# Performance work log

Measured on AMD Instinct MI355X. Metric: run time of the kernel, lower is better.

The kernel has to match this reference:

```python
import jax, jax.numpy as jnp
import numpy as np


def setup_inputs() -> dict:
    key = jax.random.key(0)
    k1, k2, k3 = jax.random.split(key, 3)
    B, C, K, W, H = 8, 512, 512, 64, 64
    x = jax.random.normal(k1, (B, C, W, H), dtype=jnp.float32)
    y = jax.random.normal(k2, (B, K, W, H), dtype=jnp.float32)
    scale = jax.random.uniform(k3, (1,), dtype=jnp.float32)
    return {"x": x, "y": y, "scale": scale}


def reference(x, y, scale):
    B, C, W, H = x.shape
    K = y.shape[1]
    xq = x.reshape(B, C, W * H)            # [B, C, N]
    yk = y.reshape(B, K, W * H)            # [B, K, N]
    # energy = Q @ K^T : [B, C, K]
    energy = jnp.einsum('bcn,bkn->bck', xq, yk)
    # inverted max-subtract softmax over last dim (K)
    energy_new = jnp.max(energy, axis=-1, keepdims=True) - energy
    attention = jax.nn.softmax(energy_new, axis=-1)  # [B, C, K]
    # out = attention @ V : [B, C, N]
    out = jnp.einsum('bck,bkn->bcn', attention, yk).reshape(B, C, W, H)
    return x + scale * out
```

## Files before the change

### kernel.cpp

```cpp
#include <hip/hip_runtime.h>
#include <hip/hip_bf16.h>
#include <stdint.h>

#define BB 8
#define CC 512
#define KK 512
#define NN 4096

typedef __bf16 bf16x8 __attribute__((ext_vector_type(8)));
typedef float f32x4 __attribute__((ext_vector_type(4)));
typedef __attribute__((address_space(3))) uint8_t* lds_ptr_t;
typedef const __attribute__((address_space(1))) uint8_t* gbl_ptr_t;

static __device__ __forceinline__ unsigned short bf16_bits(float f) {
    __bf16 h = (__bf16)f;
    return __builtin_bit_cast(unsigned short, h);
}

__global__ void __launch_bounds__(256) split_hi_lo(const float* __restrict__ in,
        unsigned short* __restrict__ hi, unsigned short* __restrict__ lo, int n4) {
    int idx = blockIdx.x * blockDim.x + threadIdx.x;
    int stride = gridDim.x * blockDim.x;
    const float4* in4 = (const float4*)in;
    ushort4* h4 = (ushort4*)hi;
    ushort4* l4 = (ushort4*)lo;
    for (int i = idx; i < n4; i += stride) {
        float4 v = in4[i];
        float a[4] = {v.x, v.y, v.z, v.w};
        unsigned short hb[4], lb[4];
        #pragma unroll
        for (int j = 0; j < 4; ++j) {
            __bf16 h = (__bf16)a[j];
            float hf = (float)h;
            __bf16 l = (__bf16)(a[j] - hf);
            hb[j] = __builtin_bit_cast(unsigned short, h);
            lb[j] = __builtin_bit_cast(unsigned short, l);
        }
        h4[i] = make_ushort4(hb[0], hb[1], hb[2], hb[3]);
        l4[i] = make_ushort4(lb[0], lb[1], lb[2], lb[3]);
    }
}

__global__ void __launch_bounds__(256) energy_gemm(
        const unsigned short* __restrict__ xh, const unsigned short* __restrict__ xl,
        const unsigned short* __restrict__ yh, const unsigned short* __restrict__ yl,
        float* __restrict__ energy) {
    __shared__ __align__(16) uint8_t smem[4 * 8192];
    const int ktile = blockIdx.x;
    const int ctile = blockIdx.y;
    const int b = blockIdx.z >> 1;
    const int half = blockIdx.z & 1;
    const int t = threadIdx.x;
    const int wave = t >> 6, lane = t & 63;

    const size_t rowB = (size_t)NN * 2;
    const uint8_t* srcBase[4];
    srcBase[0] = (const uint8_t*)xh + ((size_t)b * CC + ctile * 64) * rowB + (size_t)half * 4096;
    srcBase[1] = (const uint8_t*)xl + ((size_t)b * CC + ctile * 64) * rowB + (size_t)half * 4096;
    srcBase[2] = (const uint8_t*)yh + ((size_t)b * KK + ktile * 64) * rowB + (size_t)half * 4096;
    srcBase[3] = (const uint8_t*)yl + ((size_t)b * KK + ktile * 64) * rowB + (size_t)half * 4096;

    f32x4 acc[2][2] = {};
    const int waveRow = wave >> 1, waveCol = wave & 1;

    for (int step = 0; step < 32; ++step) {
        const size_t colByte = (size_t)step * 128;
        #pragma unroll
        for (int i = 0; i < 8; ++i) {
            const int tile = i >> 1;
            const int lc = (i & 1) * 4 + wave;
            const int u = lc * 64 + lane;
            const int r = u >> 3;
            const int c3 = (u & 7) ^ (r & 7);
            const uint8_t* src = srcBase[tile] + (size_t)r * rowB + colByte + c3 * 16;
            __builtin_amdgcn_global_load_lds((gbl_ptr_t)src,
                (lds_ptr_t)(smem + tile * 8192 + lc * 1024), 16, 0, 0);
        }
        __syncthreads();
        #pragma unroll
        for (int kf = 0; kf < 2; ++kf) {
            bf16x8 fah[2], fal[2], fbh[2], fbl[2];
            #pragma unroll
            for (int m = 0; m < 2; ++m) {
                int r = waveRow * 32 + m * 16 + (lane & 15);
                int c3 = (kf * 4 + (lane >> 4)) ^ (r & 7);
                fah[m] = *(const bf16x8*)(smem + 0 * 8192 + r * 128 + c3 * 16);
                fal[m] = *(const bf16x8*)(smem + 1 * 8192 + r * 128 + c3 * 16);
            }
            #pragma unroll
            for (int n = 0; n < 2; ++n) {
                int r = waveCol * 32 + n * 16 + (lane & 15);
                int c3 = (kf * 4 + (lane >> 4)) ^ (r & 7);
                fbh[n] = *(const bf16x8*)(smem + 2 * 8192 + r * 128 + c3 * 16);
                fbl[n] = *(const bf16x8*)(smem + 3 * 8192 + r * 128 + c3 * 16);
            }
            #pragma unroll
            for (int m = 0; m < 2; ++m)
            #pragma unroll
            for (int n = 0; n < 2; ++n) {
                acc[m][n] = __builtin_amdgcn_mfma_f32_16x16x32_bf16(fah[m], fbh[n], acc[m][n], 0, 0, 0);
                acc[m][n] = __builtin_amdgcn_mfma_f32_16x16x32_bf16(fah[m], fbl[n], acc[m][n], 0, 0, 0);
                acc[m][n] = __builtin_amdgcn_mfma_f32_16x16x32_bf16(fal[m], fbh[n], acc[m][n], 0, 0, 0);
            }
        }
        __syncthreads();
    }

    float* eout = energy + (size_t)half * BB * CC * KK + (size_t)b * CC * KK;
    const int row0 = ctile * 64 + waveRow * 32;
    const int col0 = ktile * 64 + waveCol * 32;
    #pragma unroll
    for (int m = 0; m < 2; ++m)
    #pragma unroll
    for (int n = 0; n < 2; ++n)
    #pragma unroll
    for (int j = 0; j < 4; ++j) {
        int rr = row0 + m * 16 + (lane >> 4) * 4 + j;
        int cc2 = col0 + n * 16 + (lane & 15);
        eout[(size_t)rr * KK + cc2] = acc[m][n][j];
    }
}

__global__ void __launch_bounds__(256) softmax_inv(
        const float* __restrict__ e0, const float* __restrict__ e1,
        unsigned short* __restrict__ att) {
    const int t = threadIdx.x;
    const int wave = t >> 6, lane = t & 63;
    const int row = blockIdx.x * 4 + wave;
    const float* p0 = e0 + (size_t)row * KK;
    const float* p1 = e1 + (size_t)row * KK;
    float v[8];
    float mn = 3.0e38f;
    #pragma unroll
    for (int i = 0; i < 8; ++i) {
        v[i] = p0[lane + i * 64] + p1[lane + i * 64];
        mn = fminf(mn, v[i]);
    }
    #pragma unroll
    for (int off = 32; off > 0; off >>= 1) mn = fminf(mn, __shfl_xor(mn, off));
    float p[8]; float s = 0.f;
    #pragma unroll
    for (int i = 0; i < 8; ++i) { p[i] = __expf(mn - v[i]); s += p[i]; }
    #pragma unroll
    for (int off = 32; off > 0; off >>= 1) s += __shfl_xor(s, off);
    float inv = 1.0f / s;
    unsigned short* arow = att + (size_t)row * KK;
    #pragma unroll
    for (int i = 0; i < 8; ++i) arow[lane + i * 64] = bf16_bits(p[i] * inv);
}

__global__ void __launch_bounds__(256) transpose_bf16(
        const unsigned short* __restrict__ yh, unsigned short* __restrict__ yT) {
    __shared__ unsigned short tile[64][66];
    const int n0 = blockIdx.x * 64, k0 = blockIdx.y * 64, b = blockIdx.z;
    const int t = threadIdx.x;
    const unsigned short* src = yh + (size_t)b * KK * NN;
    unsigned short* dst = yT + (size_t)b * NN * KK;
    #pragma unroll
    for (int i = 0; i < 2; ++i) {
        int idx = t + 256 * i;
        int r = idx >> 3;
        int c8 = (idx & 7) * 8;
        uint4 v = *(const uint4*)(src + (size_t)(k0 + r) * NN + n0 + c8);
        unsigned int w[4] = {v.x, v.y, v.z, v.w};
        #pragma unroll
        for (int q = 0; q < 4; ++q) {
            tile[r][c8 + 2 * q]     = (unsigned short)(w[q] & 0xffffu);
            tile[r][c8 + 2 * q + 1] = (unsigned short)(w[q] >> 16);
        }
    }
    __syncthreads();
    #pragma unroll
    for (int i = 0; i < 16; ++i) {
        int idx = t + 256 * i;
        int rn = idx >> 6;
        int ck = idx & 63;
        dst[(size_t)(n0 + rn) * KK + k0 + ck] = tile[ck][rn];
    }
}

__global__ void __launch_bounds__(256) pv_residual(
        const unsigned short* __restrict__ att, const unsigned short* __restrict__ yT,
        const float* __restrict__ x, const float* __restrict__ scale,
        float* __restrict__ out) {
    __shared__ __align__(16) uint8_t smem[2 * 16384];
    const int ntile = blockIdx.x;
    const int ctile = blockIdx.y;
    const int b = blockIdx.z;
    const int t = threadIdx.x;
    const int wave = t >> 6, lane = t & 63;
    const size_t rowB = (size_t)KK * 2;
    const uint8_t* srcA = (const uint8_t*)att + ((size_t)b * CC + ctile * 128) * rowB;
    const uint8_t* srcB = (const uint8_t*)yT  + ((size_t)b * NN + ntile * 128) * rowB;

    f32x4 acc[4][4] = {};
    const int waveRow = wave >> 1, waveCol = wave & 1;

    for (int step = 0; step < 8; ++step) {
        const size_t colByte = (size_t)step * 128;
        #pragma unroll
        for (int i = 0; i < 8; ++i) {
            const uint8_t* base = (i < 4) ? srcA : srcB;
            const int tile = i >> 2;
            const int lc = (i & 3) * 4 + wave;
            const int u = lc * 64 + lane;
            const int r = u >> 3;
            const int c3 = (u & 7) ^ (r & 7);
            const uint8_t* src = base + (size_t)r * rowB + colByte + c3 * 16;
            __builtin_amdgcn_global_load_lds((gbl_ptr_t)src,
                (lds_ptr_t)(smem + tile * 16384 + lc * 1024), 16, 0, 0);
        }
        __syncthreads();
        #pragma unroll
        for (int kf = 0; kf < 2; ++kf) {
            bf16x8 fa[4], fb[4];
            #pragma unroll
            for (int m = 0; m < 4; ++m) {
                int r = waveRow * 64 + m * 16 + (lane & 15);
                int c3 = (kf * 4 + (lane >> 4)) ^ (r & 7);
                fa[m] = *(const bf16x8*)(smem + r * 128 + c3 * 16);
            }
            #pragma unroll
            for (int n = 0; n < 4; ++n) {
                int r = waveCol * 64 + n * 16 + (lane & 15);
                int c3 = (kf * 4 + (lane >> 4)) ^ (r & 7);
                fb[n] = *(const bf16x8*)(smem + 16384 + r * 128 + c3 * 16);
            }
            #pragma unroll
            for (int m = 0; m < 4; ++m)
            #pragma unroll
            for (int n = 0; n < 4; ++n)
                acc[m][n] = __builtin_amdgcn_mfma_f32_16x16x32_bf16(fa[m], fb[n], acc[m][n], 0, 0, 0);
        }
        __syncthreads();
    }

    const float s = scale[0];
    const int row0 = ctile * 128 + waveRow * 64;
    const int col0 = ntile * 128 + waveCol * 64;
    #pragma unroll
    for (int m = 0; m < 4; ++m)
    #pragma unroll
    for (int n = 0; n < 4; ++n)
    #pragma unroll
    for (int j = 0; j < 4; ++j) {
        int rr = row0 + m * 16 + (lane >> 4) * 4 + j;
        int cc2 = col0 + n * 16 + (lane & 15);
        size_t idx = ((size_t)b * CC + rr) * NN + cc2;
        out[idx] = x[idx] + s * acc[m][n][j];
    }
}

extern "C" void kernel_launch(void* const* d_in, const int* in_sizes, int n_in,
                              void* d_out, int out_size, void* d_ws, size_t ws_size,
                              hipStream_t stream) {
    const float* x = (const float*)d_in[0];
    const float* y = (const float*)d_in[1];
    const float* scale = (const float*)d_in[2];
    float* out = (float*)d_out;
    uint8_t* ws = (uint8_t*)d_ws;
    const size_t MB = 1024 * 1024;
    unsigned short* xh = (unsigned short*)(ws + 0 * MB);
    unsigned short* xl = (unsigned short*)(ws + 32 * MB);
    unsigned short* yh = (unsigned short*)(ws + 64 * MB);
    unsigned short* yl = (unsigned short*)(ws + 96 * MB);
    float* energy = (float*)(ws + 128 * MB);
    unsigned short* yT  = (unsigned short*)(ws + 0 * MB);
    unsigned short* att = (unsigned short*)(ws + 32 * MB);

    const int n4 = BB * CC * NN / 4;
    split_hi_lo<<<4096, 256, 0, stream>>>(x, xh, xl, n4);
    split_hi_lo<<<4096, 256, 0, stream>>>(y, yh, yl, n4);
    energy_gemm<<<dim3(8, 8, BB * 2), 256, 0, stream>>>(xh, xl, yh, yl, energy);
    transpose_bf16<<<dim3(NN / 64, KK / 64, BB), 256, 0, stream>>>(yh, yT);
    softmax_inv<<<dim3(BB * CC / 4), 256, 0, stream>>>(
        energy, energy + (size_t)BB * CC * KK, att);
    pv_residual<<<dim3(NN / 128, CC / 128, BB), 256, 0, stream>>>(att, yT, x, scale, out);
}
```

Before: 323.2 us.

## Enlarge energy GEMM tile to 128x128 with 4-way split-K into output buffer

The energy GEMM tile grows from 64x64 to 128x128 per block, with each wave computing a 64x64 sub-tile. This gives more MFMA work per LDS load and halves global reloads of the bf16 hi/lo operands. The reduction dimension is split four ways instead of two, and the partial sums are staged in the output buffer rather than a separate workspace. Softmax then sums the four partials. The grid has 512 blocks, each using 64KB of LDS and 64 accumulator registers, so occupancy may drop.

```diff
diff --git a/kernel.cpp b/kernel.cpp
--- a/kernel.cpp
+++ b/kernel.cpp
@@ -44,60 +44,60 @@
 __global__ void __launch_bounds__(256) energy_gemm(
         const unsigned short* __restrict__ xh, const unsigned short* __restrict__ xl,
         const unsigned short* __restrict__ yh, const unsigned short* __restrict__ yl,
-        float* __restrict__ energy) {
-    __shared__ __align__(16) uint8_t smem[4 * 8192];
+        float* __restrict__ epart) {
+    __shared__ __align__(16) uint8_t smem[4 * 16384];
     const int ktile = blockIdx.x;
     const int ctile = blockIdx.y;
-    const int b = blockIdx.z >> 1;
-    const int half = blockIdx.z & 1;
+    const int b = blockIdx.z >> 2;
+    const int quarter = blockIdx.z & 3;
     const int t = threadIdx.x;
     const int wave = t >> 6, lane = t & 63;
 
     const size_t rowB = (size_t)NN * 2;
     const uint8_t* srcBase[4];
-    srcBase[0] = (const uint8_t*)xh + ((size_t)b * CC + ctile * 64) * rowB + (size_t)half * 4096;
-    srcBase[1] = (const uint8_t*)xl + ((size_t)b * CC + ctile * 64) * rowB + (size_t)half * 4096;
-    srcBase[2] = (const uint8_t*)yh + ((size_t)b * KK + ktile * 64) * rowB + (size_t)half * 4096;
-    srcBase[3] = (const uint8_t*)yl + ((size_t)b * KK + ktile * 64) * rowB + (size_t)half * 4096;
-
-    f32x4 acc[2][2] = {};
+    srcBase[0] = (const uint8_t*)xh + ((size_t)b * CC + ctile * 128) * rowB + (size_t)quarter * 2048;
+    srcBase[1] = (const uint8_t*)xl + ((size_t)b * CC + ctile * 128) * rowB + (size_t)quarter * 2048;
+    srcBase[2] = (const uint8_t*)yh + ((size_t)b * KK + ktile * 128) * rowB + (size_t)quarter * 2048;
+    srcBase[3] = (const uint8_t*)yl + ((size_t)b * KK + ktile * 128) * rowB + (size_t)quarter * 2048;
+
+    f32x4 acc[4][4] = {};
     const int waveRow = wave >> 1, waveCol = wave & 1;
 
-    for (int step = 0; step < 32; ++step) {
+    for (int step = 0; step < 16; ++step) {
         const size_t colByte = (size_t)step * 128;
         #pragma unroll
-        for (int i = 0; i < 8; ++i) {
-            const int tile = i >> 1;
-            const int lc = (i & 1) * 4 + wave;
+        for (int i = 0; i < 16; ++i) {
+            const int tile = i >> 2;
+            const int lc = (i & 3) * 4 + wave;
             const int u = lc * 64 + lane;
             const int r = u >> 3;
             const int c3 = (u & 7) ^ (r & 7);
             const uint8_t* src = srcBase[tile] + (size_t)r * rowB + colByte + c3 * 16;
             __builtin_amdgcn_global_load_lds((gbl_ptr_t)src,
-                (lds_ptr_t)(smem + tile * 8192 + lc * 1024), 16, 0, 0);
+                (lds_ptr_t)(smem + tile * 16384 + lc * 1024), 16, 0, 0);
         }
         __syncthreads();
         #pragma unroll
         for (int kf = 0; kf < 2; ++kf) {
-            bf16x8 fah[2], fal[2], fbh[2], fbl[2];
-            #pragma unroll
-            for (int m = 0; m < 2; ++m) {
-                int r = waveRow * 32 + m * 16 + (lane & 15);
-                int c3 = (kf * 4 + (lane >> 4)) ^ (r & 7);
-                fah[m] = *(const bf16x8*)(smem + 0 * 8192 + r * 128 + c3 * 16);
-                fal[m] = *(const bf16x8*)(smem + 1 * 8192 + r * 128 + c3 * 16);
-            }
-            #pragma unroll
-            for (int n = 0; n < 2; ++n) {
-                int r = waveCol * 32 + n * 16 + (lane & 15);
-                int c3 = (kf * 4 + (lane >> 4)) ^ (r & 7);
-                fbh[n] = *(const bf16x8*)(smem + 2 * 8192 + r * 128 + c3 * 16);
-                fbl[n] = *(const bf16x8*)(smem + 3 * 8192 + r * 128 + c3 * 16);
-            }
-            #pragma unroll
-            for (int m = 0; m < 2; ++m)
-            #pragma unroll
-            for (int n = 0; n < 2; ++n) {
+            bf16x8 fah[4], fal[4], fbh[4], fbl[4];
+            #pragma unroll
+            for (int m = 0; m < 4; ++m) {
+                int r = waveRow * 64 + m * 16 + (lane & 15);
+                int c3 = (kf * 4 + (lane >> 4)) ^ (r & 7);
+                fah[m] = *(const bf16x8*)(smem + 0 * 16384 + r * 128 + c3 * 16);
+                fal[m] = *(const bf16x8*)(smem + 1 * 16384 + r * 128 + c3 * 16);
+            }
+            #pragma unroll
+            for (int n = 0; n < 4; ++n) {
+                int r = waveCol * 64 + n * 16 + (lane & 15);
+                int c3 = (kf * 4 + (lane >> 4)) ^ (r & 7);
+                fbh[n] = *(const bf16x8*)(smem + 2 * 16384 + r * 128 + c3 * 16);
+                fbl[n] = *(const bf16x8*)(smem + 3 * 16384 + r * 128 + c3 * 16);
+            }
+            #pragma unroll
+            for (int m = 0; m < 4; ++m)
+            #pragma unroll
+            for (int n = 0; n < 4; ++n) {
                 acc[m][n] = __builtin_amdgcn_mfma_f32_16x16x32_bf16(fah[m], fbh[n], acc[m][n], 0, 0, 0);
                 acc[m][n] = __builtin_amdgcn_mfma_f32_16x16x32_bf16(fah[m], fbl[n], acc[m][n], 0, 0, 0);
                 acc[m][n] = __builtin_amdgcn_mfma_f32_16x16x32_bf16(fal[m], fbh[n], acc[m][n], 0, 0, 0);
@@ -106,13 +106,13 @@
         __syncthreads();
     }
 
-    float* eout = energy + (size_t)half * BB * CC * KK + (size_t)b * CC * KK;
-    const int row0 = ctile * 64 + waveRow * 32;
-    const int col0 = ktile * 64 + waveCol * 32;
-    #pragma unroll
-    for (int m = 0; m < 2; ++m)
-    #pragma unroll
-    for (int n = 0; n < 2; ++n)
+    float* eout = epart + (size_t)quarter * BB * CC * KK + (size_t)b * CC * KK;
+    const int row0 = ctile * 128 + waveRow * 64;
+    const int col0 = ktile * 128 + waveCol * 64;
+    #pragma unroll
+    for (int m = 0; m < 4; ++m)
+    #pragma unroll
+    for (int n = 0; n < 4; ++n)
     #pragma unroll
     for (int j = 0; j < 4; ++j) {
         int rr = row0 + m * 16 + (lane >> 4) * 4 + j;
@@ -122,18 +122,18 @@
 }
 
 __global__ void __launch_bounds__(256) softmax_inv(
-        const float* __restrict__ e0, const float* __restrict__ e1,
-        unsigned short* __restrict__ att) {
+        const float* __restrict__ e, unsigned short* __restrict__ att) {
     const int t = threadIdx.x;
     const int wave = t >> 6, lane = t & 63;
     const int row = blockIdx.x * 4 + wave;
-    const float* p0 = e0 + (size_t)row * KK;
-    const float* p1 = e1 + (size_t)row * KK;
+    const size_t Q = (size_t)BB * CC * KK;
+    const float* p0 = e + (size_t)row * KK;
     float v[8];
     float mn = 3.0e38f;
     #pragma unroll
     for (int i = 0; i < 8; ++i) {
-        v[i] = p0[lane + i * 64] + p1[lane + i * 64];
+        int c = lane + i * 64;
+        v[i] = p0[c] + p0[Q + c] + p0[2 * Q + c] + p0[3 * Q + c];
         mn = fminf(mn, v[i]);
     }
     #pragma unroll
@@ -264,16 +264,15 @@
     unsigned short* xl = (unsigned short*)(ws + 32 * MB);
     unsigned short* yh = (unsigned short*)(ws + 64 * MB);
     unsigned short* yl = (unsigned short*)(ws + 96 * MB);
-    float* energy = (float*)(ws + 128 * MB);
+    float* epart = out;
     unsigned short* yT  = (unsigned short*)(ws + 0 * MB);
     unsigned short* att = (unsigned short*)(ws + 32 * MB);
 
     const int n4 = BB * CC * NN / 4;
     split_hi_lo<<<4096, 256, 0, stream>>>(x, xh, xl, n4);
     split_hi_lo<<<4096, 256, 0, stream>>>(y, yh, yl, n4);
-    energy_gemm<<<dim3(8, 8, BB * 2), 256, 0, stream>>>(xh, xl, yh, yl, energy);
+    energy_gemm<<<dim3(4, 4, BB * 4), 256, 0, stream>>>(xh, xl, yh, yl, epart);
     transpose_bf16<<<dim3(NN / 64, KK / 64, BB), 256, 0, stream>>>(yh, yT);
-    softmax_inv<<<dim3(BB * CC / 4), 256, 0, stream>>>(
-        energy, energy + (size_t)BB * CC * KK, att);
+    softmax_inv<<<dim3(BB * CC / 4), 256, 0, stream>>>(epart, att);
     pv_residual<<<dim3(NN / 128, CC / 128, BB), 256, 0, stream>>>(att, yT, x, scale, out);
 }
```

Result: faster. 302.3 us (-6.5%).
